# Performance work log

Hardware: AMD Instinct MI355X
Metric: run time of the kernel (lower is better)

The kernel has to match this reference:

```python
import jax, jax.numpy as jnp
import numpy as np

S, B, T = 16, 32, 64        # max_sents, batch, max_tokens
V, E, H = 50000, 256, 256   # vocab, embed_size, gru_hidden (n_dim)
NC = 50                     # n_classes


def setup_inputs() -> dict:
    key = jax.random.key(0)
    ks = jax.random.split(key, 30)

    def u(k, shape, s=0.1):
        return jax.random.uniform(k, shape, minval=-s, maxval=s, dtype=jnp.float32)

    return {
        "x": jax.random.randint(ks[0], (S, B, T), 0, V, dtype=jnp.int64),
        "embed": jax.random.normal(ks[1], (V, E), dtype=jnp.float32) * 0.1,
        # word-level bi-GRU (input E, hidden H); gate order r,z,n as in torch
        "wg_Wih_f": u(ks[2], (3 * H, E)), "wg_Whh_f": u(ks[3], (3 * H, H)),
        "wg_bih_f": u(ks[4], (3 * H,)),   "wg_bhh_f": u(ks[5], (3 * H,)),
        "wg_Wih_b": u(ks[6], (3 * H, E)), "wg_Whh_b": u(ks[7], (3 * H, H)),
        "wg_bih_b": u(ks[8], (3 * H,)),   "wg_bhh_b": u(ks[9], (3 * H,)),
        "word_W": u(ks[10], (2 * H, 2 * H)),
        "word_b": u(ks[11], (2 * H, 1)),
        "word_proj": u(ks[12], (2 * H, 1)),
        # sentence-level bi-GRU (input 2H, hidden H)
        "sg_Wih_f": u(ks[13], (3 * H, 2 * H)), "sg_Whh_f": u(ks[14], (3 * H, H)),
        "sg_bih_f": u(ks[15], (3 * H,)),       "sg_bhh_f": u(ks[16], (3 * H,)),
        "sg_Wih_b": u(ks[17], (3 * H, 2 * H)), "sg_Whh_b": u(ks[18], (3 * H, H)),
        "sg_bih_b": u(ks[19], (3 * H,)),       "sg_bhh_b": u(ks[20], (3 * H,)),
        "sent_W": u(ks[21], (2 * H, 2 * H)),
        "sent_b": u(ks[22], (2 * H, 1)),
        "sent_proj": u(ks[23], (2 * H, 1)),
        "fin_W": u(ks[24], (NC, 2 * H)),
        "fin_b": u(ks[25], (NC,)),
        "state_word": jnp.zeros((2, B, H), dtype=jnp.float32),
        "state_sent": jnp.zeros((2, B, H), dtype=jnp.float32),
    }


def _gru_dir(x, h0, Wih, Whh, bih, bhh, reverse=False):
    # x: [T, B, in]; returns hidden states [T, B, H] (in original time order)
    xp = jnp.einsum('tbe,ge->tbg', x, Wih) + bih  # precompute input projections

    def step(h, xt):
        g = h @ Whh.T + bhh
        xr, xz, xn = jnp.split(xt, 3, axis=-1)
        hr, hz, hn = jnp.split(g, 3, axis=-1)
        r = jax.nn.sigmoid(xr + hr)
        z = jax.nn.sigmoid(xz + hz)
        n = jnp.tanh(xn + r * hn)
        h = (1.0 - z) * n + z * h
        return h, h

    _, hs = jax.lax.scan(step, h0, xp, reverse=reverse)
    return hs


def _bigru(x, h0, Wf, Hf, bif, bhf, Wb, Hb, bib, bhb):
    f = _gru_dir(x, h0[0], Wf, Hf, bif, bhf, reverse=False)
    b = _gru_dir(x, h0[1], Wb, Hb, bib, bhb, reverse=True)
    return jnp.concatenate([f, b], axis=-1)  # [T, B, 2H]


def _attn_pool(out, W, b, proj):
    # out: [T, B, 2H]; batch_matmul_bias(tanh) -> batch_matmul -> softmax over T -> weighted sum
    squish = jnp.tanh(jnp.einsum('tbh,hk->tbk', out, W) + b[:, 0])  # [T,B,2H]
    scores = jnp.einsum('tbk,k->tb', squish, proj[:, 0])            # [T,B]
    a = jax.nn.softmax(scores, axis=0)                              # softmax over seq
    return jnp.einsum('tb,tbh->bh', a, out)                         # [B,2H]


def reference(x, embed,
              wg_Wih_f, wg_Whh_f, wg_bih_f, wg_bhh_f,
              wg_Wih_b, wg_Whh_b, wg_bih_b, wg_bhh_b,
              word_W, word_b, word_proj,
              sg_Wih_f, sg_Whh_f, sg_bih_f, sg_bhh_f,
              sg_Wih_b, sg_Whh_b, sg_bih_b, sg_bhh_b,
              sent_W, sent_b, sent_proj,
              fin_W, fin_b, state_word, state_sent):
    e = embed[x]                         # [S,B,T,E]
    e = jnp.transpose(e, (0, 2, 1, 3))   # [S,T,B,E] (torch code transposes per sentence)

    word_out = jax.vmap(
        lambda xs: _bigru(xs, state_word,
                          wg_Wih_f, wg_Whh_f, wg_bih_f, wg_bhh_f,
                          wg_Wih_b, wg_Whh_b, wg_bih_b, wg_bhh_b)
    )(e)                                 # [S,T,B,2H]

    s = jax.vmap(lambda o: _attn_pool(o, word_W, word_b, word_proj))(word_out)  # [S,B,2H]

    sent_out = _bigru(s, state_sent,
                      sg_Wih_f, sg_Whh_f, sg_bih_f, sg_bhh_f,
                      sg_Wih_b, sg_Whh_b, sg_bih_b, sg_bhh_b)  # [S,B,2H]
    pooled = _attn_pool(sent_out, sent_W, sent_b, sent_proj)   # [B,2H]
    return pooled @ fin_W.T + fin_b                            # [B,NC] logits
```

## Files before the change

### kernel.cpp

```cpp
#include <hip/hip_runtime.h>


typedef float  f32x4  __attribute__((ext_vector_type(4)));
typedef int    i32x4  __attribute__((ext_vector_type(4)));
typedef __bf16 bf16x8 __attribute__((ext_vector_type(8)));

#define DEVINL static __device__ __forceinline__

DEVINL unsigned short f2bf(float f) {
    unsigned int x = __builtin_bit_cast(unsigned int, f);
    x = x + 0x7fffu + ((x >> 16) & 1u);
    return (unsigned short)(x >> 16);
}
DEVINL float bf2f(unsigned short u) {
    unsigned int x = ((unsigned int)u) << 16;
    return __builtin_bit_cast(float, x);
}
DEVINL float bfe16(unsigned int v, int hi) {
    return bf2f((unsigned short)(hi ? (v >> 16) : (v & 0xffffu)));
}
DEVINL float sigm(float x) { return __builtin_amdgcn_rcpf(1.f + __expf(-x)); }
DEVINL float tanh_(float x) {
    x = fminf(fmaxf(x, -20.f), 20.f);
    float e = __expf(-2.f * x);
    return (1.f - e) * __builtin_amdgcn_rcpf(1.f + e);
}
DEVINL void mfma16(f32x4& acc, i32x4 a, i32x4 b) {
    acc = __builtin_amdgcn_mfma_f32_16x16x32_bf16(
        __builtin_bit_cast(bf16x8, a), __builtin_bit_cast(bf16x8, b), acc, 0, 0, 0);
}
DEVINL f32x4 zero4() { f32x4 v = {0.f, 0.f, 0.f, 0.f}; return v; }

#define O_WPWF    ((size_t)0)
#define O_WPWB    ((size_t)1048576)
#define O_WPSGIH  ((size_t)2097152)
#define O_WPSHHF  ((size_t)3670016)
#define O_WPSHHB  ((size_t)4063232)
#define O_WPWW    ((size_t)4456448)
#define O_WPSW    ((size_t)4980736)
#define O_BIASWF  ((size_t)5505024)
#define O_BIASWB  ((size_t)5509120)
#define O_BIHCAT  ((size_t)5513216)
#define O_WOUT    ((size_t)5519360)
#define O_SCORESW ((size_t)39073792)
#define O_SSFRAG  ((size_t)39204864)
#define O_XPSENT  ((size_t)39729152)
#define O_SOFRAG  ((size_t)42874880)
#define O_SCORESS ((size_t)43399168)
#define WS_NEED_B ((size_t)43401216)
#define O_XPW     ((size_t)43401216)
#define WS_NEED_A ((size_t)144064512)

__global__ void k_prep(const float* wihf, const float* whhf,
                       const float* wihb, const float* whhb,
                       const float* sgihf, const float* sgihb,
                       const float* sghhf, const float* sghhb,
                       const float* wordW, const float* sentW,
                       const float* bihf, const float* bhhf,
                       const float* bihb, const float* bhhb,
                       const float* sgbihf, const float* sgbihb,
                       const float* sgbhhf, const float* sgbhhb,
                       unsigned short* Wpwf, unsigned short* Wpwb,
                       unsigned short* Wpsgih,
                       unsigned short* WpshhF, unsigned short* WpshhB,
                       unsigned short* WpwW, unsigned short* WpsW,
                       float* biasWf, float* biasWb, float* bihCat)
{
    const int tid0 = blockIdx.x * blockDim.x + threadIdx.x;
    const int nth  = gridDim.x * blockDim.x;

    for (int idx = tid0; idx < 2 * 524288; idx += nth) {
        int d = idx >> 19, sidx = idx & 524287;
        int j = sidx & 7, chunk = sidx >> 3;
        int lane = chunk & 63, nk = chunk >> 6;
        int kf = nk & 15, nf = nk >> 4;
        int n = nf * 16 + (lane & 15);
        int k = kf * 32 + (lane >> 4) * 8 + j;
        const float* Wih = d ? wihb : wihf;
        const float* Whh = d ? whhb : whhf;
        int g4 = n >> 8, jj = n & 255;
        float v = 0.f;
        if (k < 256) {
            if (g4 == 0) v = Wih[jj * 256 + k];
            else if (g4 == 1) v = Wih[(256 + jj) * 256 + k];
            else if (g4 == 2) v = Wih[(512 + jj) * 256 + k];
        } else {
            int kk = k - 256;
            if (g4 == 0) v = Whh[jj * 256 + kk];
            else if (g4 == 1) v = Whh[(256 + jj) * 256 + kk];
            else if (g4 == 3) v = Whh[(512 + jj) * 256 + kk];
        }
        (d ? Wpwb : Wpwf)[sidx] = f2bf(v);
    }
    for (int idx = tid0; idx < 786432; idx += nth) {
        int j = idx & 7, chunk = idx >> 3;
        int lane = chunk & 63, nk = chunk >> 6;
        int kf = nk & 15, nf = nk >> 4;
        int n = nf * 16 + (lane & 15);
        int k = kf * 32 + (lane >> 4) * 8 + j;
        float v = (n < 768) ? sgihf[n * 512 + k] : sgihb[(n - 768) * 512 + k];
        Wpsgih[idx] = f2bf(v);
    }
    for (int idx = tid0; idx < 2 * 196608; idx += nth) {
        int d = idx >= 196608;
        int sidx = d ? idx - 196608 : idx;
        int j = sidx & 7, chunk = sidx >> 3;
        int lane = chunk & 63, nk = chunk >> 6;
        int kf = nk & 7, nf = nk >> 3;
        int n = nf * 16 + (lane & 15);
        int k = kf * 32 + (lane >> 4) * 8 + j;
        float v = (d ? sghhb : sghhf)[n * 256 + k];
        (d ? WpshhB : WpshhF)[sidx] = f2bf(v);
    }
    for (int idx = tid0; idx < 2 * 262144; idx += nth) {
        int d = idx >> 18, sidx = idx & 262143;
        int j = sidx & 7, chunk = sidx >> 3;
        int lane = chunk & 63, nk = chunk >> 6;
        int kf = nk & 15, nf = nk >> 4;
        int n = nf * 16 + (lane & 15);
        int k = kf * 32 + (lane >> 4) * 8 + j;
        float v = (d ? sentW : wordW)[k * 512 + n];
        (d ? WpsW : WpwW)[sidx] = f2bf(v);
    }
    for (int idx = tid0; idx < 2048; idx += nth) {
        int d = idx >> 10, i = idx & 1023;
        int g4 = i >> 8, j = i & 255;
        const float* bi = d ? bihb : bihf;
        const float* bh = d ? bhhb : bhhf;
        float v = (g4 == 0) ? bi[j] + bh[j]
                : (g4 == 1) ? bi[256 + j] + bh[256 + j]
                : (g4 == 2) ? bi[512 + j] : bh[512 + j];
        (d ? biasWb : biasWf)[i] = v;
    }
    for (int idx = tid0; idx < 1536; idx += nth) {
        int d = idx >= 768, j = d ? idx - 768 : idx;
        const float* bi = d ? sgbihb : sgbihf;
        const float* bh = d ? sgbhhb : sgbhhf;
        bihCat[idx] = bi[j] + ((j < 512) ? bh[j] : 0.f);
    }
}

__global__ __launch_bounds__(512, 2)
void k_xpw(const int* xg, const float* embed,
           const unsigned short* Wpwf_u, const unsigned short* Wpwb_u,
           const float* biasWf, const float* biasWb, unsigned short* xpw)
{
    __shared__ unsigned short Ebuf[2][16][256];
    const int tid = threadIdx.x, lane = tid & 63, w = tid >> 6;
    const int cid = blockIdx.x;
    const int tq = cid & 3, bh = (cid >> 2) & 1, dir = (cid >> 3) & 1, s = cid >> 4;
    const int t0 = tq * 16;
    const i32x4* Wp = (const i32x4*)(dir ? Wpwb_u : Wpwf_u);
    const float* biasW = dir ? biasWb : biasWf;
    const int b = lane & 15, rsub = lane >> 4;

    i32x4 A[3][2][8];
#pragma unroll
    for (int g = 0; g < 3; ++g)
#pragma unroll
        for (int q = 0; q < 2; ++q)
#pragma unroll
            for (int kk = 0; kk < 8; ++kk)
                A[g][q][kk] = Wp[((g * 16 + w * 2 + q) * 16 + kk) * 64 + lane];

    unsigned int biasp[3][2][2];
#pragma unroll
    for (int g = 0; g < 3; ++g)
#pragma unroll
        for (int q = 0; q < 2; ++q) {
            const int j0 = g * 256 + (w * 2 + q) * 16 + rsub * 4;
            biasp[g][q][0] = (unsigned)f2bf(biasW[j0]) |
                             ((unsigned)f2bf(biasW[j0 + 1]) << 16);
            biasp[g][q][1] = (unsigned)f2bf(biasW[j0 + 2]) |
                             ((unsigned)f2bf(biasW[j0 + 3]) << 16);
        }

    const int sb = tid >> 5, sc = tid & 31;
    const int tokrow = (s * 32 + bh * 16 + sb) * 64;
    const int sdst = sb * 512 + ((sc * 16) ^ ((sb & 7) << 4));

#define STAGE_E(BUF, T)                                                       \
    {                                                                         \
        const int tok = xg[tokrow + (T)];                                     \
        const f32x4* src = (const f32x4*)(embed + (size_t)tok * 256 + sc * 8);\
        f32x4 e0 = src[0], e1 = src[1];                                       \
        i32x4 pk;                                                             \
        pk.x = (int)((unsigned)f2bf(e0.x) | ((unsigned)f2bf(e0.y) << 16));    \
        pk.y = (int)((unsigned)f2bf(e0.z) | ((unsigned)f2bf(e0.w) << 16));    \
        pk.z = (int)((unsigned)f2bf(e1.x) | ((unsigned)f2bf(e1.y) << 16));    \
        pk.w = (int)((unsigned)f2bf(e1.z) | ((unsigned)f2bf(e1.w) << 16));    \
        *(i32x4*)((char*)&Ebuf[BUF][0][0] + sdst) = pk;                       \
    }

    STAGE_E(0, t0);
    const size_t chain = (size_t)((s * 2 + dir) * 2 + bh);
    char* const xpBase = (char*)xpw + chain * 1572864 +
                         (size_t)(rsub * 128 + b * 8);

    for (int tl = 0; tl < 16; ++tl) {
        __syncthreads();
        const int t = t0 + tl, cur = tl & 1, nxt = cur ^ 1;
        if (tl < 15) STAGE_E(nxt, t + 1);

        f32x4 acc[3][2];
#pragma unroll
        for (int g = 0; g < 3; ++g) { acc[g][0] = zero4(); acc[g][1] = zero4(); }
#pragma unroll
        for (int kk = 0; kk < 8; ++kk) {
            const int roff = b * 512 + ((kk * 64 + rsub * 16) ^ ((b & 7) << 4));
            i32x4 eb = *(const i32x4*)((const char*)&Ebuf[cur][0][0] + roff);
            mfma16(acc[0][0], A[0][0][kk], eb); mfma16(acc[0][1], A[0][1][kk], eb);
            mfma16(acc[1][0], A[1][0][kk], eb); mfma16(acc[1][1], A[1][1][kk], eb);
            mfma16(acc[2][0], A[2][0][kk], eb); mfma16(acc[2][1], A[2][1][kk], eb);
        }
        char* ob = xpBase + (size_t)t * 24576;
#pragma unroll
        for (int g = 0; g < 3; ++g)
#pragma unroll
            for (int q = 0; q < 2; ++q) {
                unsigned short us[4];
#pragma unroll
                for (int i = 0; i < 4; ++i)
                    us[i] = f2bf(acc[g][q][i] + bfe16(biasp[g][q][i >> 1], i & 1));
                uint2 pk;
                pk.x = (unsigned)us[0] | ((unsigned)us[1] << 16);
                pk.y = (unsigned)us[2] | ((unsigned)us[3] << 16);
                *(uint2*)(ob + g * 8192 + (w * 2 + q) * 512) = pk;
            }
    }
#undef STAGE_E
}

__global__ __launch_bounds__(512, 2)
void k_gru_wordA(const float* stateW,
                 const unsigned short* Wpwf_u, const unsigned short* Wpwb_u,
                 const float* biasWf, const float* biasWb,
                 const unsigned short* xpw, unsigned short* wout)
{
    __shared__ unsigned short Hbuf[2][16][256];
    const int tid = threadIdx.x, lane = tid & 63, w = tid >> 6;
    const int cid = blockIdx.x, bh = cid & 1, dir = (cid >> 1) & 1, s = cid >> 2;
    const i32x4* Wp = (const i32x4*)(dir ? Wpwb_u : Wpwf_u);
    const float* biasW = dir ? biasWb : biasWf;
    const int b = lane & 15, rsub = lane >> 4;
    const int gmap[3] = {0, 1, 3};

    i32x4 A[3][2][8];
#pragma unroll
    for (int g = 0; g < 3; ++g)
#pragma unroll
        for (int q = 0; q < 2; ++q)
#pragma unroll
            for (int kk = 0; kk < 8; ++kk)
                A[g][q][kk] =
                    Wp[((gmap[g] * 16 + w * 2 + q) * 16 + 8 + kk) * 64 + lane];

    unsigned int bhnp[2][2];
    float hreg[2][4];
#pragma unroll
    for (int q = 0; q < 2; ++q) {
        const int j0 = (w * 2 + q) * 16 + rsub * 4;
        f32x4 h0 = *(const f32x4*)(stateW + dir * 8192 + (bh * 16 + b) * 256 + j0);
        bhnp[q][0] = (unsigned)f2bf(biasW[768 + j0]) |
                     ((unsigned)f2bf(biasW[768 + j0 + 1]) << 16);
        bhnp[q][1] = (unsigned)f2bf(biasW[768 + j0 + 2]) |
                     ((unsigned)f2bf(biasW[768 + j0 + 3]) << 16);
        hreg[q][0] = h0.x; hreg[q][1] = h0.y; hreg[q][2] = h0.z; hreg[q][3] = h0.w;
        uint2 pk;
        pk.x = (unsigned)f2bf(h0.x) | ((unsigned)f2bf(h0.y) << 16);
        pk.y = (unsigned)f2bf(h0.z) | ((unsigned)f2bf(h0.w) << 16);
        const int boff = b * 512 + (((w * 2 + q) * 32 + rsub * 8) ^ ((b & 7) << 4));
        *(uint2*)((char*)&Hbuf[0][0][0] + boff) = pk;
    }
    const size_t chain = (size_t)((s * 2 + dir) * 2 + bh);
    const char* const xpBase = (const char*)xpw + chain * 1572864 +
                               (size_t)(rsub * 128 + b * 8);

    for (int ti = 0; ti < 64; ++ti) {
        __syncthreads();
        const int t = dir ? 63 - ti : ti;
        const int cur = ti & 1, nxt = cur ^ 1;

        uint2 xpv[3][2];
        const char* xb = xpBase + (size_t)t * 24576;
#pragma unroll
        for (int g = 0; g < 3; ++g)
#pragma unroll
            for (int q = 0; q < 2; ++q)
                xpv[g][q] = *(const uint2*)(xb + g * 8192 + (w * 2 + q) * 512);

        f32x4 acc[3][2];
#pragma unroll
        for (int g = 0; g < 3; ++g) { acc[g][0] = zero4(); acc[g][1] = zero4(); }
#pragma unroll
        for (int kk = 0; kk < 8; ++kk) {
            const int roff = b * 512 + ((kk * 64 + rsub * 16) ^ ((b & 7) << 4));
            i32x4 hb = *(const i32x4*)((const char*)&Hbuf[cur][0][0] + roff);
            mfma16(acc[0][0], A[0][0][kk], hb); mfma16(acc[0][1], A[0][1][kk], hb);
            mfma16(acc[1][0], A[1][0][kk], hb); mfma16(acc[1][1], A[1][1][kk], hb);
            mfma16(acc[2][0], A[2][0][kk], hb); mfma16(acc[2][1], A[2][1][kk], hb);
        }
        const int r = (s * 64 + t) * 32 + bh * 16 + b;
#pragma unroll
        for (int q = 0; q < 2; ++q) {
            unsigned short us[4];
#pragma unroll
            for (int i = 0; i < 4; ++i) {
                const unsigned xr = (i < 2) ? xpv[0][q].x : xpv[0][q].y;
                const unsigned xz = (i < 2) ? xpv[1][q].x : xpv[1][q].y;
                const unsigned xn = (i < 2) ? xpv[2][q].x : xpv[2][q].y;
                float rv = sigm(bfe16(xr, i & 1) + acc[0][q][i]);
                float zv = sigm(bfe16(xz, i & 1) + acc[1][q][i]);
                float nv = tanh_(bfe16(xn, i & 1) +
                                 rv * (acc[2][q][i] + bfe16(bhnp[q][i >> 1], i & 1)));
                float h = (1.f - zv) * nv + zv * hreg[q][i];
                hreg[q][i] = h;
                us[i] = f2bf(h);
            }
            uint2 pk;
            pk.x = (unsigned)us[0] | ((unsigned)us[1] << 16);
            pk.y = (unsigned)us[2] | ((unsigned)us[3] << 16);
            const int boff = b * 512 + (((w * 2 + q) * 32 + rsub * 8) ^ ((b & 7) << 4));
            *(uint2*)((char*)&Hbuf[nxt][0][0] + boff) = pk;
            const int hcol = dir * 256 + (w * 2 + q) * 16 + rsub * 4;
            const int widx = (((r >> 4) * 16 + (hcol >> 5)) * 64 + (r & 15) +
                              ((hcol >> 3) & 3) * 16) * 8 + (hcol & 7);
            *(uint2*)(wout + widx) = pk;
        }
    }
}

DEVINL void prefetchE(unsigned short (*Ab)[512], const int* xg, const float* embed,
                      int s, int t, int tid)
{
    const int brow = tid >> 5, c = tid & 31;
    const int tok = xg[(s * 32 + brow) * 64 + t];
    const f32x4* src = (const f32x4*)(embed + (size_t)tok * 256) + c * 2;
    f32x4 f0 = src[0], f1 = src[1];
    i32x4 pk;
    pk.x = (int)((unsigned)f2bf(f0.x) | ((unsigned)f2bf(f0.y) << 16));
    pk.y = (int)((unsigned)f2bf(f0.z) | ((unsigned)f2bf(f0.w) << 16));
    pk.z = (int)((unsigned)f2bf(f1.x) | ((unsigned)f2bf(f1.y) << 16));
    pk.w = (int)((unsigned)f2bf(f1.z) | ((unsigned)f2bf(f1.w) << 16));
    int kbyte = (c * 16) ^ ((brow & 7) << 4);
    *(i32x4*)((char*)&Ab[brow][0] + kbyte) = pk;
}

__global__ __launch_bounds__(1024, 4)
void k_gru_word(const int* xg, const float* embed, const float* stateW,
                const unsigned short* Wpwf_u, const unsigned short* Wpwb_u,
                const float* biasWf, const float* biasWb,
                unsigned short* wout)
{
    __shared__ unsigned short Abuf[2][32][512];
    const int tid = threadIdx.x, lane = tid & 63, w = tid >> 6;
    const int cid = blockIdx.x, s = cid >> 1, dir = cid & 1;
    const i32x4* Wp = (const i32x4*)(dir ? Wpwb_u : Wpwf_u);
    const float* bias = dir ? biasWb : biasWf;

    const int j = w * 16 + (lane & 15);
    float hreg[2][4];
#pragma unroll
    for (int mf = 0; mf < 2; ++mf)
#pragma unroll
        for (int i = 0; i < 4; ++i) {
            int b = mf * 16 + (lane >> 4) * 4 + i;
            float h0 = stateW[dir * 8192 + b * 256 + j];
            hreg[mf][i] = h0;
            int byteoff = ((256 + j) * 2) ^ ((b & 7) << 4);
            *(unsigned short*)((char*)&Abuf[0][b][0] + byteoff) = f2bf(h0);
        }
    const int tfirst = dir ? 63 : 0;
    prefetchE(Abuf[0], xg, embed, s, tfirst, tid);

    const float br = bias[j], bz = bias[256 + j];
    const float bxn = bias[512 + j], bhn = bias[768 + j];

    for (int ti = 0; ti < 64; ++ti) {
        __syncthreads();
        const int t = dir ? 63 - ti : ti;
        const int cur = ti & 1, nxt = cur ^ 1;
        if (ti < 63) prefetchE(Abuf[nxt], xg, embed, s, dir ? t - 1 : t + 1, tid);

        f32x4 acc[4][2];
#pragma unroll
        for (int g = 0; g < 4; ++g) { acc[g][0] = zero4(); acc[g][1] = zero4(); }

        i32x4 bbuf[3][3];
#define LOADB_W(KF, DST)                                                     \
        {                                                                    \
            const int gX = ((KF) < 8) ? 32 : 48;                             \
            DST[0] = Wp[((0 + w)  * 16 + (KF)) * 64 + lane];                 \
            DST[1] = Wp[((16 + w) * 16 + (KF)) * 64 + lane];                 \
            DST[2] = Wp[((gX + w) * 16 + (KF)) * 64 + lane];                 \
        }
        LOADB_W(0, bbuf[0]);
        LOADB_W(1, bbuf[1]);
#pragma unroll
        for (int kf = 0; kf < 16; ++kf) {
            if (kf < 14) LOADB_W(kf + 2, bbuf[(kf + 2) % 3]);
            const int row0 = lane & 15;
            const int boff = (kf * 64 + (lane >> 4) * 16) ^ ((row0 & 7) << 4);
            i32x4 a0 = *(const i32x4*)((const char*)&Abuf[cur][row0][0] + boff);
            i32x4 a1 = *(const i32x4*)((const char*)&Abuf[cur][16 + row0][0] + boff);
            const i32x4* bc = bbuf[kf % 3];
            mfma16(acc[0][0], a0, bc[0]); mfma16(acc[0][1], a1, bc[0]);
            mfma16(acc[1][0], a0, bc[1]); mfma16(acc[1][1], a1, bc[1]);
            if (kf < 8) { mfma16(acc[2][0], a0, bc[2]);
                          mfma16(acc[2][1], a1, bc[2]); }
            else        { mfma16(acc[3][0], a0, bc[2]);
                          mfma16(acc[3][1], a1, bc[2]); }
        }
#undef LOADB_W
#pragma unroll
        for (int mf = 0; mf < 2; ++mf)
#pragma unroll
            for (int i = 0; i < 4; ++i) {
                const int b = mf * 16 + (lane >> 4) * 4 + i;
                float rv = sigm(acc[0][mf][i] + br);
                float zv = sigm(acc[1][mf][i] + bz);
                float nv = tanh_(acc[2][mf][i] + bxn + rv * (acc[3][mf][i] + bhn));
                float hnew = (1.f - zv) * nv + zv * hreg[mf][i];
                hreg[mf][i] = hnew;
                unsigned short hb = f2bf(hnew);
                int byteoff = ((256 + j) * 2) ^ ((b & 7) << 4);
                *(unsigned short*)((char*)&Abuf[nxt][b][0] + byteoff) = hb;
                int r = (s * 64 + t) * 32 + b;
                int hcol = dir * 256 + j;
                wout[(((r >> 4) * 16 + (hcol >> 5)) * 64 + (r & 15) +
                      ((hcol >> 3) & 3) * 16) * 8 + (hcol & 7)] = hb;
            }
    }
}

__global__ __launch_bounds__(1024, 4)
void k_attn_score2(const unsigned short* Afrag_u, const unsigned short* Wp_u,
                   const float* wb, const float* wp, float* scores)
{
    __shared__ i32x4 Wl[2][16][64];
    const int tid = threadIdx.x, lane = tid & 63, w = tid >> 6;
    const int rblk = blockIdx.x * 16 + w;
    const i32x4* A = (const i32x4*)Afrag_u;
    const i32x4* Wg = (const i32x4*)Wp_u;

    i32x4 a[16];
#pragma unroll
    for (int kf = 0; kf < 16; ++kf) a[kf] = A[(rblk * 16 + kf) * 64 + lane];

    i32x4* wl0 = &Wl[0][0][0];
    i32x4* wl1 = &Wl[1][0][0];
    wl0[tid] = Wg[tid];

    float partial[4] = {};
    for (int nf = 0; nf < 32; ++nf) {
        __syncthreads();
        if (nf < 31) {
            i32x4* dst = (nf & 1) ? wl0 : wl1;
            dst[tid] = Wg[(nf + 1) * 1024 + tid];
        }
        const i32x4* cur = (nf & 1) ? wl1 : wl0;
        f32x4 acc0 = zero4(), acc1 = zero4();
#pragma unroll
        for (int kf = 0; kf < 16; kf += 2) {
            mfma16(acc0, a[kf],     cur[kf * 64 + lane]);
            mfma16(acc1, a[kf + 1], cur[(kf + 1) * 64 + lane]);
        }
        const int n = nf * 16 + (lane & 15);
        const float wbn = wb[n], wpn = wp[n];
#pragma unroll
        for (int i = 0; i < 4; ++i)
            partial[i] += tanh_(acc0[i] + acc1[i] + wbn) * wpn;
    }
#pragma unroll
    for (int i = 0; i < 4; ++i) {
        float v = partial[i];
        v += __shfl_xor(v, 1); v += __shfl_xor(v, 2);
        v += __shfl_xor(v, 4); v += __shfl_xor(v, 8);
        if ((lane & 15) == 0)
            scores[rblk * 16 + (lane >> 4) * 4 + i] = v;
    }
}

__global__ void k_attn_score_small(const unsigned short* Afrag_u,
                                   const unsigned short* Wp_u,
                                   const float* wb, const float* wp, float* scores)
{
    const int tid = threadIdx.x, lane = tid & 63, w = tid >> 6;
    const int rblk = blockIdx.x * 4 + w;
    const i32x4* A = (const i32x4*)Afrag_u;
    const i32x4* Wp = (const i32x4*)Wp_u;
    i32x4 a[16];
#pragma unroll
    for (int kf = 0; kf < 16; ++kf) a[kf] = A[(rblk * 16 + kf) * 64 + lane];

    float partial[4] = {};
    for (int nf = 0; nf < 32; ++nf) {
        f32x4 acc0 = zero4(), acc1 = zero4();
#pragma unroll
        for (int kf = 0; kf < 16; kf += 2) {
            mfma16(acc0, a[kf],     Wp[(nf * 16 + kf) * 64 + lane]);
            mfma16(acc1, a[kf + 1], Wp[(nf * 16 + kf + 1) * 64 + lane]);
        }
        const int n = nf * 16 + (lane & 15);
        const float wbn = wb[n], wpn = wp[n];
#pragma unroll
        for (int i = 0; i < 4; ++i)
            partial[i] += tanh_(acc0[i] + acc1[i] + wbn) * wpn;
    }
#pragma unroll
    for (int i = 0; i < 4; ++i) {
        float v = partial[i];
        v += __shfl_xor(v, 1); v += __shfl_xor(v, 2);
        v += __shfl_xor(v, 4); v += __shfl_xor(v, 8);
        if ((lane & 15) == 0)
            scores[rblk * 16 + (lane >> 4) * 4 + i] = v;
    }
}

__global__ void k_word_pool(const float* scores, const unsigned short* wout,
                            unsigned short* ssFrag)
{
    __shared__ float aL[64];
    __shared__ float part[4][64][8];
    const int tid = threadIdx.x, l = tid & 63, w = tid >> 6;
    const int bid = blockIdx.x;
    const int s = bid >> 5, b = bid & 31;
    if (w == 0) {
        float sc = scores[s * 2048 + l * 32 + b];
        float m = sc;
#pragma unroll
        for (int d = 1; d < 64; d <<= 1) m = fmaxf(m, __shfl_xor(m, d));
        float e = __expf(sc - m), sum = e;
#pragma unroll
        for (int d = 1; d < 64; d <<= 1) sum += __shfl_xor(sum, d);
        aL[l] = e * __builtin_amdgcn_rcpf(sum);
    }
    __syncthreads();

    float acc[8] = {};
    const i32x4* WO = (const i32x4*)wout;
    for (int tt = 0; tt < 16; ++tt) {
        const int t = w * 16 + tt;
        float at = aL[t];
        int cidx = ((s * 128 + t * 2 + (b >> 4)) * 16 + (l >> 2)) * 64 +
                   (b & 15) + (l & 3) * 16;
        i32x4 ch = WO[cidx];
        acc[0] += at * bf2f((unsigned short)((unsigned)ch.x & 0xffffu));
        acc[1] += at * bf2f((unsigned short)((unsigned)ch.x >> 16));
        acc[2] += at * bf2f((unsigned short)((unsigned)ch.y & 0xffffu));
        acc[3] += at * bf2f((unsigned short)((unsigned)ch.y >> 16));
        acc[4] += at * bf2f((unsigned short)((unsigned)ch.z & 0xffffu));
        acc[5] += at * bf2f((unsigned short)((unsigned)ch.z >> 16));
        acc[6] += at * bf2f((unsigned short)((unsigned)ch.w & 0xffffu));
        acc[7] += at * bf2f((unsigned short)((unsigned)ch.w >> 16));
    }
#pragma unroll
    for (int q = 0; q < 8; ++q) part[w][l][q] = acc[q];
    __syncthreads();
    if (w == 0) {
        float fin[8];
#pragma unroll
        for (int q = 0; q < 8; ++q)
            fin[q] = part[0][l][q] + part[1][l][q] + part[2][l][q] + part[3][l][q];
        i32x4 pk;
        pk.x = (int)((unsigned)f2bf(fin[0]) | ((unsigned)f2bf(fin[1]) << 16));
        pk.y = (int)((unsigned)f2bf(fin[2]) | ((unsigned)f2bf(fin[3]) << 16));
        pk.z = (int)((unsigned)f2bf(fin[4]) | ((unsigned)f2bf(fin[5]) << 16));
        pk.w = (int)((unsigned)f2bf(fin[6]) | ((unsigned)f2bf(fin[7]) << 16));
        const int r2 = s * 32 + b;
        int cidx2 = ((r2 >> 4) * 16 + (l >> 2)) * 64 + (r2 & 15) + (l & 3) * 16;
        ((i32x4*)ssFrag)[cidx2] = pk;
    }
}

__global__ void k_sgih(const unsigned short* ssFrag_u, const unsigned short* Wp_u,
                       const float* bihCat, float* xpSent)
{
    const int tid = threadIdx.x, lane = tid & 63, w = tid >> 6;
    const int rblk = blockIdx.x, ncl = blockIdx.y;
    const i32x4* A = (const i32x4*)ssFrag_u;
    const i32x4* Wp = (const i32x4*)Wp_u;
    i32x4 a[16];
#pragma unroll
    for (int kf = 0; kf < 16; ++kf) a[kf] = A[(rblk * 16 + kf) * 64 + lane];
#pragma unroll
    for (int nfl = 0; nfl < 4; ++nfl) {
        const int nfg = ncl * 16 + w * 4 + nfl;
        f32x4 acc = zero4();
#pragma unroll
        for (int kf = 0; kf < 16; ++kf)
            mfma16(acc, a[kf], Wp[(nfg * 16 + kf) * 64 + lane]);
        const int n = nfg * 16 + (lane & 15);
        const float bb = bihCat[n];
        const int dir = n >= 768, ng = n - dir * 768;
        const int g = ng >> 8, jj = ng & 255;
#pragma unroll
        for (int i = 0; i < 4; ++i) {
            int row = rblk * 16 + (lane >> 4) * 4 + i;
            int s = row >> 5, b = row & 31;
            xpSent[(((dir * 2 + (b >> 4)) * 16 + s) * 12288) +
                   (g * 256 + jj) * 16 + (b & 15)] = acc[i] + bb;
        }
    }
}

DEVINL void gload16(const void* gsrc, void* ldst) {
    __builtin_amdgcn_global_load_lds(
        (const __attribute__((address_space(1))) unsigned int*)gsrc,
        (__attribute__((address_space(3))) unsigned int*)ldst, 16, 0, 0);
}

__global__ __launch_bounds__(512)
void k_gru_sentA(const float* stateS, const unsigned short* WpF_u,
                 const unsigned short* WpB_u, const float* bhhf, const float* bhhb,
                 const float* xpSent, unsigned short* soFrag)
{
    __shared__ unsigned short Abuf[2][16][256];
    __shared__ float xpLs[2][12288];
    const int tid = threadIdx.x, lane = tid & 63, w = tid >> 6;
    const int cid = blockIdx.x, bh = cid & 1, dir = cid >> 1;
    const i32x4* Wp = (const i32x4*)(dir ? WpB_u : WpF_u);
    const float* bhh = dir ? bhhb : bhhf;

    i32x4 B[3][2][8];
#pragma unroll
    for (int g = 0; g < 3; ++g)
#pragma unroll
        for (int q = 0; q < 2; ++q)
#pragma unroll
            for (int kk = 0; kk < 8; ++kk)
                B[g][q][kk] = Wp[((g * 16 + w * 2 + q) * 8 + kk) * 64 + lane];

    float bhn[2];
    float hreg[2][4];
#pragma unroll
    for (int q = 0; q < 2; ++q) {
        const int j = (w * 2 + q) * 16 + (lane & 15);
        bhn[q] = bhh[512 + j];
#pragma unroll
        for (int i = 0; i < 4; ++i) {
            const int b = 4 * (lane >> 4) + i;
            float h0 = stateS[dir * 8192 + (bh * 16 + b) * 256 + j];
            hreg[q][i] = h0;
            int byteoff = b * 512 + ((j * 2) ^ ((b & 7) << 4));
            *(unsigned short*)((char*)&Abuf[0][0][0] + byteoff) = f2bf(h0);
        }
    }
    const size_t xbase = (size_t)((dir * 2 + bh) * 16) * 49152;
    const int sfirst = dir ? 15 : 0;
#pragma unroll
    for (int c = 0; c < 6; ++c)
        gload16((const char*)xpSent + xbase + (size_t)sfirst * 49152 +
                    ((w * 6 + c) * 64 + lane) * 16,
                (char*)&xpLs[0][0] + (w * 6 + c) * 1024);

    for (int si = 0; si < 16; ++si) {
        __syncthreads();
        const int s = dir ? 15 - si : si;
        const int cur = si & 1, nxt = cur ^ 1;
        if (si < 15) {
            const int sn = dir ? s - 1 : s + 1;
#pragma unroll
            for (int c = 0; c < 6; ++c)
                gload16((const char*)xpSent + xbase + (size_t)sn * 49152 +
                            ((w * 6 + c) * 64 + lane) * 16,
                        (char*)&xpLs[nxt][0] + (w * 6 + c) * 1024);
        }
        f32x4 acc[3][2];
#pragma unroll
        for (int g = 0; g < 3; ++g) { acc[g][0] = zero4(); acc[g][1] = zero4(); }
#pragma unroll
        for (int kk = 0; kk < 8; ++kk) {
            const int row = lane & 15;
            const int boff = (kk * 64 + (lane >> 4) * 16) ^ ((row & 7) << 4);
            i32x4 a = *(const i32x4*)((const char*)&Abuf[cur][row][0] + boff);
#pragma unroll
            for (int g = 0; g < 3; ++g) {
                mfma16(acc[g][0], a, B[g][0][kk]);
                mfma16(acc[g][1], a, B[g][1][kk]);
            }
        }
#pragma unroll
        for (int q = 0; q < 2; ++q) {
            const int j = (w * 2 + q) * 16 + (lane & 15);
            f32x4 xr = *(const f32x4*)((const char*)&xpLs[cur][0] +
                        ((0 * 256 + j) * 16 + 4 * (lane >> 4)) * 4);
            f32x4 xz = *(const f32x4*)((const char*)&xpLs[cur][0] +
                        ((1 * 256 + j) * 16 + 4 * (lane >> 4)) * 4);
            f32x4 xn = *(const f32x4*)((const char*)&xpLs[cur][0] +
                        ((2 * 256 + j) * 16 + 4 * (lane >> 4)) * 4);
#pragma unroll
            for (int i = 0; i < 4; ++i) {
                const int b = 4 * (lane >> 4) + i;
                float rv = sigm(xr[i] + acc[0][q][i]);
                float zv = sigm(xz[i] + acc[1][q][i]);
                float nv = tanh_(xn[i] + rv * (acc[2][q][i] + bhn[q]));
                float hnew = (1.f - zv) * nv + zv * hreg[q][i];
                hreg[q][i] = hnew;
                unsigned short hb = f2bf(hnew);
                int byteoff = b * 512 + ((j * 2) ^ ((b & 7) << 4));
                *(unsigned short*)((char*)&Abuf[nxt][0][0] + byteoff) = hb;
                const int r2 = s * 32 + bh * 16 + b;
                const int hcol = dir * 256 + j;
                soFrag[(((r2 >> 4) * 16 + (hcol >> 5)) * 64 + (r2 & 15) +
                        ((hcol >> 3) & 3) * 16) * 8 + (hcol & 7)] = hb;
            }
        }
    }
}

__global__ void k_sent_pool_fin(const float* scoresS, const unsigned short* soFrag,
                                const float* finW, const float* finb, float* out)
{
    __shared__ float aL[16];
    __shared__ float pooled[512];
    __shared__ float part[4][64];
    const int l = threadIdx.x;
    const int b = blockIdx.x;

    if (l < 64) {
        float sc = (l < 16) ? scoresS[l * 32 + b] : -1e30f;
        float m = sc;
#pragma unroll
        for (int d = 1; d < 16; d <<= 1) m = fmaxf(m, __shfl_xor(m, d));
        float e = (l < 16) ? __expf(sc - m) : 0.f;
        float sum = e;
#pragma unroll
        for (int d = 1; d < 16; d <<= 1) sum += __shfl_xor(sum, d);
        if (l < 16) aL[l] = e * __builtin_amdgcn_rcpf(sum);
    }
    __syncthreads();

    if (l < 64) {
        float acc[8] = {};
        const i32x4* SO = (const i32x4*)soFrag;
        for (int si = 0; si < 16; ++si) {
            float as = aL[si];
            int r2 = si * 32 + b;
            int cidx = ((r2 >> 4) * 16 + (l >> 2)) * 64 + (r2 & 15) + (l & 3) * 16;
            i32x4 ch = SO[cidx];
            acc[0] += as * bf2f((unsigned short)((unsigned)ch.x & 0xffffu));
            acc[1] += as * bf2f((unsigned short)((unsigned)ch.x >> 16));
            acc[2] += as * bf2f((unsigned short)((unsigned)ch.y & 0xffffu));
            acc[3] += as * bf2f((unsigned short)((unsigned)ch.y >> 16));
            acc[4] += as * bf2f((unsigned short)((unsigned)ch.z & 0xffffu));
            acc[5] += as * bf2f((unsigned short)((unsigned)ch.z >> 16));
            acc[6] += as * bf2f((unsigned short)((unsigned)ch.w & 0xffffu));
            acc[7] += as * bf2f((unsigned short)((unsigned)ch.w >> 16));
        }
#pragma unroll
        for (int q = 0; q < 8; ++q) pooled[l * 8 + q] = acc[q];
    }
    __syncthreads();
    {
        const int c = l & 63, kq = l >> 6;
        float v = 0.f;
        if (c < 50) {
            const float* wrow = finW + c * 512 + kq * 128;
            const float* pp = pooled + kq * 128;
            for (int k = 0; k < 128; ++k) v += pp[k] * wrow[k];
        }
        part[kq][c] = v;
    }
    __syncthreads();
    if (l < 50)
        out[b * 50 + l] = finb[l] + part[0][l] + part[1][l] + part[2][l] + part[3][l];
}

extern "C" void kernel_launch(void* const* d_in, const int* in_sizes, int n_in,
                              void* d_out, int out_size, void* d_ws, size_t ws_size,
                              hipStream_t stream)
{
    if (ws_size < WS_NEED_B) return;
    const int bigA = (ws_size >= WS_NEED_A) ? 1 : 0;

    const int*   x      = (const int*)d_in[0];
    const float* embed  = (const float*)d_in[1];
    const float* wgWihF = (const float*)d_in[2];
    const float* wgWhhF = (const float*)d_in[3];
    const float* wgBihF = (const float*)d_in[4];
    const float* wgBhhF = (const float*)d_in[5];
    const float* wgWihB = (const float*)d_in[6];
    const float* wgWhhB = (const float*)d_in[7];
    const float* wgBihB = (const float*)d_in[8];
    const float* wgBhhB = (const float*)d_in[9];
    const float* wordW  = (const float*)d_in[10];
    const float* wordB  = (const float*)d_in[11];
    const float* wordP  = (const float*)d_in[12];
    const float* sgWihF = (const float*)d_in[13];
    const float* sgWhhF = (const float*)d_in[14];
    const float* sgBihF = (const float*)d_in[15];
    const float* sgBhhF = (const float*)d_in[16];
    const float* sgWihB = (const float*)d_in[17];
    const float* sgWhhB = (const float*)d_in[18];
    const float* sgBihB = (const float*)d_in[19];
    const float* sgBhhB = (const float*)d_in[20];
    const float* sentWm = (const float*)d_in[21];
    const float* sentB  = (const float*)d_in[22];
    const float* sentP  = (const float*)d_in[23];
    const float* finW   = (const float*)d_in[24];
    const float* finB   = (const float*)d_in[25];
    const float* stateW = (const float*)d_in[26];
    const float* stateS = (const float*)d_in[27];

    char* ws = (char*)d_ws;
    unsigned short* Wpwf   = (unsigned short*)(ws + O_WPWF);
    unsigned short* Wpwb   = (unsigned short*)(ws + O_WPWB);
    unsigned short* Wpsgih = (unsigned short*)(ws + O_WPSGIH);
    unsigned short* WpshhF = (unsigned short*)(ws + O_WPSHHF);
    unsigned short* WpshhB = (unsigned short*)(ws + O_WPSHHB);
    unsigned short* WpwW   = (unsigned short*)(ws + O_WPWW);
    unsigned short* WpsW   = (unsigned short*)(ws + O_WPSW);
    float* biasWf  = (float*)(ws + O_BIASWF);
    float* biasWb  = (float*)(ws + O_BIASWB);
    float* bihCat  = (float*)(ws + O_BIHCAT);
    unsigned short* wout   = (unsigned short*)(ws + O_WOUT);
    float* scoresW = (float*)(ws + O_SCORESW);
    unsigned short* ssFrag = (unsigned short*)(ws + O_SSFRAG);
    float* xpSent  = (float*)(ws + O_XPSENT);
    unsigned short* soFrag = (unsigned short*)(ws + O_SOFRAG);
    float* scoresS = (float*)(ws + O_SCORESS);
    unsigned short* xpw    = (unsigned short*)(ws + O_XPW);

    k_prep<<<512, 256, 0, stream>>>(wgWihF, wgWhhF, wgWihB, wgWhhB,
                                    sgWihF, sgWihB, sgWhhF, sgWhhB,
                                    wordW, sentWm,
                                    wgBihF, wgBhhF, wgBihB, wgBhhB,
                                    sgBihF, sgBihB, sgBhhF, sgBhhB,
                                    Wpwf, Wpwb, Wpsgih, WpshhF, WpshhB,
                                    WpwW, WpsW, biasWf, biasWb, bihCat);

    if (bigA) {
        k_xpw<<<256, 512, 0, stream>>>(x, embed, Wpwf, Wpwb, biasWf, biasWb, xpw);
        k_gru_wordA<<<64, 512, 0, stream>>>(stateW, Wpwf, Wpwb, biasWf, biasWb,
                                            xpw, wout);
    } else {
        k_gru_word<<<32, 1024, 0, stream>>>(x, embed, stateW, Wpwf, Wpwb,
                                            biasWf, biasWb, wout);
    }

    k_attn_score2<<<128, 1024, 0, stream>>>(wout, WpwW, wordB, wordP, scoresW);
    k_word_pool<<<512, 256, 0, stream>>>(scoresW, wout, ssFrag);

    k_sgih<<<dim3(32, 6), 256, 0, stream>>>(ssFrag, Wpsgih, bihCat, xpSent);
    k_gru_sentA<<<4, 512, 0, stream>>>(stateS, WpshhF, WpshhB, sgBhhF, sgBhhB,
                                       xpSent, soFrag);

    k_attn_score_small<<<8, 256, 0, stream>>>(soFrag, WpsW, sentB, sentP, scoresS);
    k_sent_pool_fin<<<32, 256, 0, stream>>>(scoresS, soFrag, finW, finB,
                                            (float*)d_out);
}
```

Measured before the change: 445.2 us.

## Double waves per block in recurrent GRU kernels, one 16-column tile per wave

The word-level and sentence-level recurrent GRU kernels now launch 1024 threads (16 waves) instead of 512. Each wave handles one 16-wide hidden tile rather than two, which halves the serial MFMA chain and gate math per wave on every time step. This also halves each wave's register-resident weight fragments. The cost is a larger block barrier each step and lower occupancy, since only one block fits per CU. The change also switches f2bf to the native bf16 conversion and rewrites the hidden-state update as nv + z*(h-nv).

```diff
diff --git a/kernel.cpp b/kernel.cpp
--- a/kernel.cpp
+++ b/kernel.cpp
@@ -8,9 +8,8 @@
 #define DEVINL static __device__ __forceinline__
 
 DEVINL unsigned short f2bf(float f) {
-    unsigned int x = __builtin_bit_cast(unsigned int, f);
-    x = x + 0x7fffu + ((x >> 16) & 1u);
-    return (unsigned short)(x >> 16);
+    __bf16 b = (__bf16)f;
+    return __builtin_bit_cast(unsigned short, b);
 }
 DEVINL float bf2f(unsigned short u) {
     unsigned int x = ((unsigned int)u) << 16;
@@ -231,7 +230,7 @@
 #undef STAGE_E
 }
 
-__global__ __launch_bounds__(512, 2)
+__global__ __launch_bounds__(1024)
 void k_gru_wordA(const float* stateW,
                  const unsigned short* Wpwf_u, const unsigned short* Wpwb_u,
                  const float* biasWf, const float* biasWb,
@@ -245,31 +244,28 @@
     const int b = lane & 15, rsub = lane >> 4;
     const int gmap[3] = {0, 1, 3};
 
-    i32x4 A[3][2][8];
+    i32x4 A[3][8];
 #pragma unroll
     for (int g = 0; g < 3; ++g)
 #pragma unroll
-        for (int q = 0; q < 2; ++q)
-#pragma unroll
-            for (int kk = 0; kk < 8; ++kk)
-                A[g][q][kk] =
-                    Wp[((gmap[g] * 16 + w * 2 + q) * 16 + 8 + kk) * 64 + lane];
-
-    unsigned int bhnp[2][2];
-    float hreg[2][4];
-#pragma unroll
-    for (int q = 0; q < 2; ++q) {
-        const int j0 = (w * 2 + q) * 16 + rsub * 4;
+        for (int kk = 0; kk < 8; ++kk)
+            A[g][kk] = Wp[((gmap[g] * 16 + w) * 16 + 8 + kk) * 64 + lane];
+
+    const int j0 = w * 16 + rsub * 4;
+    unsigned int bhnp[2];
+    bhnp[0] = (unsigned)f2bf(biasW[768 + j0]) |
+              ((unsigned)f2bf(biasW[768 + j0 + 1]) << 16);
+    bhnp[1] = (unsigned)f2bf(biasW[768 + j0 + 2]) |
+              ((unsigned)f2bf(biasW[768 + j0 + 3]) << 16);
+
+    const int boff = b * 512 + ((w * 32 + rsub * 8) ^ ((b & 7) << 4));
+    float hreg[4];
+    {
         f32x4 h0 = *(const f32x4*)(stateW + dir * 8192 + (bh * 16 + b) * 256 + j0);
-        bhnp[q][0] = (unsigned)f2bf(biasW[768 + j0]) |
-                     ((unsigned)f2bf(biasW[768 + j0 + 1]) << 16);
-        bhnp[q][1] = (unsigned)f2bf(biasW[768 + j0 + 2]) |
-                     ((unsigned)f2bf(biasW[768 + j0 + 3]) << 16);
-        hreg[q][0] = h0.x; hreg[q][1] = h0.y; hreg[q][2] = h0.z; hreg[q][3] = h0.w;
+        hreg[0] = h0.x; hreg[1] = h0.y; hreg[2] = h0.z; hreg[3] = h0.w;
         uint2 pk;
         pk.x = (unsigned)f2bf(h0.x) | ((unsigned)f2bf(h0.y) << 16);
         pk.y = (unsigned)f2bf(h0.z) | ((unsigned)f2bf(h0.w) << 16);
-        const int boff = b * 512 + (((w * 2 + q) * 32 + rsub * 8) ^ ((b & 7) << 4));
         *(uint2*)((char*)&Hbuf[0][0][0] + boff) = pk;
     }
     const size_t chain = (size_t)((s * 2 + dir) * 2 + bh);
@@ -281,52 +277,46 @@
         const int t = dir ? 63 - ti : ti;
         const int cur = ti & 1, nxt = cur ^ 1;
 
-        uint2 xpv[3][2];
+        uint2 xpv[3];
         const char* xb = xpBase + (size_t)t * 24576;
 #pragma unroll
         for (int g = 0; g < 3; ++g)
-#pragma unroll
-            for (int q = 0; q < 2; ++q)
-                xpv[g][q] = *(const uint2*)(xb + g * 8192 + (w * 2 + q) * 512);
-
-        f32x4 acc[3][2];
-#pragma unroll
-        for (int g = 0; g < 3; ++g) { acc[g][0] = zero4(); acc[g][1] = zero4(); }
+            xpv[g] = *(const uint2*)(xb + g * 8192 + w * 512);
+
+        f32x4 acc[3];
+#pragma unroll
+        for (int g = 0; g < 3; ++g) acc[g] = zero4();
 #pragma unroll
         for (int kk = 0; kk < 8; ++kk) {
             const int roff = b * 512 + ((kk * 64 + rsub * 16) ^ ((b & 7) << 4));
             i32x4 hb = *(const i32x4*)((const char*)&Hbuf[cur][0][0] + roff);
-            mfma16(acc[0][0], A[0][0][kk], hb); mfma16(acc[0][1], A[0][1][kk], hb);
-            mfma16(acc[1][0], A[1][0][kk], hb); mfma16(acc[1][1], A[1][1][kk], hb);
-            mfma16(acc[2][0], A[2][0][kk], hb); mfma16(acc[2][1], A[2][1][kk], hb);
+            mfma16(acc[0], A[0][kk], hb);
+            mfma16(acc[1], A[1][kk], hb);
+            mfma16(acc[2], A[2][kk], hb);
         }
         const int r = (s * 64 + t) * 32 + bh * 16 + b;
-#pragma unroll
-        for (int q = 0; q < 2; ++q) {
-            unsigned short us[4];
-#pragma unroll
-            for (int i = 0; i < 4; ++i) {
-                const unsigned xr = (i < 2) ? xpv[0][q].x : xpv[0][q].y;
-                const unsigned xz = (i < 2) ? xpv[1][q].x : xpv[1][q].y;
-                const unsigned xn = (i < 2) ? xpv[2][q].x : xpv[2][q].y;
-                float rv = sigm(bfe16(xr, i & 1) + acc[0][q][i]);
-                float zv = sigm(bfe16(xz, i & 1) + acc[1][q][i]);
-                float nv = tanh_(bfe16(xn, i & 1) +
-                                 rv * (acc[2][q][i] + bfe16(bhnp[q][i >> 1], i & 1)));
-                float h = (1.f - zv) * nv + zv * hreg[q][i];
-                hreg[q][i] = h;
-                us[i] = f2bf(h);
-            }
-            uint2 pk;
-            pk.x = (unsigned)us[0] | ((unsigned)us[1] << 16);
-            pk.y = (unsigned)us[2] | ((unsigned)us[3] << 16);
-            const int boff = b * 512 + (((w * 2 + q) * 32 + rsub * 8) ^ ((b & 7) << 4));
-            *(uint2*)((char*)&Hbuf[nxt][0][0] + boff) = pk;
-            const int hcol = dir * 256 + (w * 2 + q) * 16 + rsub * 4;
-            const int widx = (((r >> 4) * 16 + (hcol >> 5)) * 64 + (r & 15) +
-                              ((hcol >> 3) & 3) * 16) * 8 + (hcol & 7);
-            *(uint2*)(wout + widx) = pk;
-        }
+        unsigned short us[4];
+#pragma unroll
+        for (int i = 0; i < 4; ++i) {
+            const unsigned xr = (i < 2) ? xpv[0].x : xpv[0].y;
+            const unsigned xz = (i < 2) ? xpv[1].x : xpv[1].y;
+            const unsigned xn = (i < 2) ? xpv[2].x : xpv[2].y;
+            float rv = sigm(bfe16(xr, i & 1) + acc[0][i]);
+            float zv = sigm(bfe16(xz, i & 1) + acc[1][i]);
+            float nv = tanh_(bfe16(xn, i & 1) +
+                             rv * (acc[2][i] + bfe16(bhnp[i >> 1], i & 1)));
+            float h = nv + zv * (hreg[i] - nv);
+            hreg[i] = h;
+            us[i] = f2bf(h);
+        }
+        uint2 pk;
+        pk.x = (unsigned)us[0] | ((unsigned)us[1] << 16);
+        pk.y = (unsigned)us[2] | ((unsigned)us[3] << 16);
+        *(uint2*)((char*)&Hbuf[nxt][0][0] + boff) = pk;
+        const int hcol = dir * 256 + j0;
+        const int widx = (((r >> 4) * 16 + (hcol >> 5)) * 64 + (r & 15) +
+                          ((hcol >> 3) & 3) * 16) * 8 + (hcol & 7);
+        *(uint2*)(wout + widx) = pk;
     }
 }
 
@@ -610,7 +600,7 @@
         (__attribute__((address_space(3))) unsigned int*)ldst, 16, 0, 0);
 }
 
-__global__ __launch_bounds__(512)
+__global__ __launch_bounds__(1024)
 void k_gru_sentA(const float* stateS, const unsigned short* WpF_u,
                  const unsigned short* WpB_u, const float* bhhf, const float* bhhb,
                  const float* xpSent, unsigned short* soFrag)
@@ -622,37 +612,31 @@
     const i32x4* Wp = (const i32x4*)(dir ? WpB_u : WpF_u);
     const float* bhh = dir ? bhhb : bhhf;
 
-    i32x4 B[3][2][8];
+    i32x4 B[3][8];
 #pragma unroll
     for (int g = 0; g < 3; ++g)
 #pragma unroll
-        for (int q = 0; q < 2; ++q)
-#pragma unroll
-            for (int kk = 0; kk < 8; ++kk)
-                B[g][q][kk] = Wp[((g * 16 + w * 2 + q) * 8 + kk) * 64 + lane];
-
-    float bhn[2];
-    float hreg[2][4];
-#pragma unroll
-    for (int q = 0; q < 2; ++q) {
-        const int j = (w * 2 + q) * 16 + (lane & 15);
-        bhn[q] = bhh[512 + j];
-#pragma unroll
-        for (int i = 0; i < 4; ++i) {
-            const int b = 4 * (lane >> 4) + i;
-            float h0 = stateS[dir * 8192 + (bh * 16 + b) * 256 + j];
-            hreg[q][i] = h0;
-            int byteoff = b * 512 + ((j * 2) ^ ((b & 7) << 4));
-            *(unsigned short*)((char*)&Abuf[0][0][0] + byteoff) = f2bf(h0);
-        }
+        for (int kk = 0; kk < 8; ++kk)
+            B[g][kk] = Wp[((g * 16 + w) * 8 + kk) * 64 + lane];
+
+    const int j = w * 16 + (lane & 15);
+    const float bhn = bhh[512 + j];
+    float hreg[4];
+#pragma unroll
+    for (int i = 0; i < 4; ++i) {
+        const int b = 4 * (lane >> 4) + i;
+        float h0 = stateS[dir * 8192 + (bh * 16 + b) * 256 + j];
+        hreg[i] = h0;
+        int byteoff = b * 512 + ((j * 2) ^ ((b & 7) << 4));
+        *(unsigned short*)((char*)&Abuf[0][0][0] + byteoff) = f2bf(h0);
     }
     const size_t xbase = (size_t)((dir * 2 + bh) * 16) * 49152;
     const int sfirst = dir ? 15 : 0;
 #pragma unroll
-    for (int c = 0; c < 6; ++c)
+    for (int c = 0; c < 3; ++c)
         gload16((const char*)xpSent + xbase + (size_t)sfirst * 49152 +
-                    ((w * 6 + c) * 64 + lane) * 16,
-                (char*)&xpLs[0][0] + (w * 6 + c) * 1024);
+                    ((w * 3 + c) * 64 + lane) * 16,
+                (char*)&xpLs[0][0] + (w * 3 + c) * 1024);
 
     for (int si = 0; si < 16; ++si) {
         __syncthreads();
@@ -661,50 +645,44 @@
         if (si < 15) {
             const int sn = dir ? s - 1 : s + 1;
 #pragma unroll
-            for (int c = 0; c < 6; ++c)
+            for (int c = 0; c < 3; ++c)
                 gload16((const char*)xpSent + xbase + (size_t)sn * 49152 +
-                            ((w * 6 + c) * 64 + lane) * 16,
-                        (char*)&xpLs[nxt][0] + (w * 6 + c) * 1024);
-        }
-        f32x4 acc[3][2];
-#pragma unroll
-        for (int g = 0; g < 3; ++g) { acc[g][0] = zero4(); acc[g][1] = zero4(); }
+                            ((w * 3 + c) * 64 + lane) * 16,
+                        (char*)&xpLs[nxt][0] + (w * 3 + c) * 1024);
+        }
+        f32x4 acc[3];
+#pragma unroll
+        for (int g = 0; g < 3; ++g) acc[g] = zero4();
 #pragma unroll
         for (int kk = 0; kk < 8; ++kk) {
             const int row = lane & 15;
             const int boff = (kk * 64 + (lane >> 4) * 16) ^ ((row & 7) << 4);
             i32x4 a = *(const i32x4*)((const char*)&Abuf[cur][row][0] + boff);
-#pragma unroll
-            for (int g = 0; g < 3; ++g) {
-                mfma16(acc[g][0], a, B[g][0][kk]);
-                mfma16(acc[g][1], a, B[g][1][kk]);
-            }
-        }
-#pragma unroll
-        for (int q = 0; q < 2; ++q) {
-            const int j = (w * 2 + q) * 16 + (lane & 15);
-            f32x4 xr = *(const f32x4*)((const char*)&xpLs[cur][0] +
-                        ((0 * 256 + j) * 16 + 4 * (lane >> 4)) * 4);
-            f32x4 xz = *(const f32x4*)((const char*)&xpLs[cur][0] +
-                        ((1 * 256 + j) * 16 + 4 * (lane >> 4)) * 4);
-            f32x4 xn = *(const f32x4*)((const char*)&xpLs[cur][0] +
-                        ((2 * 256 + j) * 16 + 4 * (lane >> 4)) * 4);
-#pragma unroll
-            for (int i = 0; i < 4; ++i) {
-                const int b = 4 * (lane >> 4) + i;
-                float rv = sigm(xr[i] + acc[0][q][i]);
-                float zv = sigm(xz[i] + acc[1][q][i]);
-                float nv = tanh_(xn[i] + rv * (acc[2][q][i] + bhn[q]));
-                float hnew = (1.f - zv) * nv + zv * hreg[q][i];
-                hreg[q][i] = hnew;
-                unsigned short hb = f2bf(hnew);
-                int byteoff = b * 512 + ((j * 2) ^ ((b & 7) << 4));
-                *(unsigned short*)((char*)&Abuf[nxt][0][0] + byteoff) = hb;
-                const int r2 = s * 32 + bh * 16 + b;
-                const int hcol = dir * 256 + j;
-                soFrag[(((r2 >> 4) * 16 + (hcol >> 5)) * 64 + (r2 & 15) +
-                        ((hcol >> 3) & 3) * 16) * 8 + (hcol & 7)] = hb;
-            }
+            mfma16(acc[0], a, B[0][kk]);
+            mfma16(acc[1], a, B[1][kk]);
+            mfma16(acc[2], a, B[2][kk]);
+        }
+        f32x4 xr = *(const f32x4*)((const char*)&xpLs[cur][0] +
+                    ((0 * 256 + j) * 16 + 4 * (lane >> 4)) * 4);
+        f32x4 xz = *(const f32x4*)((const char*)&xpLs[cur][0] +
+                    ((1 * 256 + j) * 16 + 4 * (lane >> 4)) * 4);
+        f32x4 xn = *(const f32x4*)((const char*)&xpLs[cur][0] +
+                    ((2 * 256 + j) * 16 + 4 * (lane >> 4)) * 4);
+#pragma unroll
+        for (int i = 0; i < 4; ++i) {
+            const int b = 4 * (lane >> 4) + i;
+            float rv = sigm(xr[i] + acc[0][i]);
+            float zv = sigm(xz[i] + acc[1][i]);
+            float nv = tanh_(xn[i] + rv * (acc[2][i] + bhn));
+            float hnew = nv + zv * (hreg[i] - nv);
+            hreg[i] = hnew;
+            unsigned short hb = f2bf(hnew);
+            int byteoff = b * 512 + ((j * 2) ^ ((b & 7) << 4));
+            *(unsigned short*)((char*)&Abuf[nxt][0][0] + byteoff) = hb;
+            const int r2 = s * 32 + bh * 16 + b;
+            const int hcol = dir * 256 + j;
+            soFrag[(((r2 >> 4) * 16 + (hcol >> 5)) * 64 + (r2 & 15) +
+                    ((hcol >> 3) & 3) * 16) * 8 + (hcol & 7)] = hb;
         }
     }
 }
@@ -832,8 +810,8 @@
 
     if (bigA) {
         k_xpw<<<256, 512, 0, stream>>>(x, embed, Wpwf, Wpwb, biasWf, biasWb, xpw);
-        k_gru_wordA<<<64, 512, 0, stream>>>(stateW, Wpwf, Wpwb, biasWf, biasWb,
-                                            xpw, wout);
+        k_gru_wordA<<<64, 1024, 0, stream>>>(stateW, Wpwf, Wpwb, biasWf, biasWb,
+                                             xpw, wout);
     } else {
         k_gru_word<<<32, 1024, 0, stream>>>(x, embed, stateW, Wpwf, Wpwb,
                                             biasWf, biasWb, wout);
@@ -843,8 +821,8 @@
     k_word_pool<<<512, 256, 0, stream>>>(scoresW, wout, ssFrag);
 
     k_sgih<<<dim3(32, 6), 256, 0, stream>>>(ssFrag, Wpsgih, bihCat, xpSent);
-    k_gru_sentA<<<4, 512, 0, stream>>>(stateS, WpshhF, WpshhB, sgBhhF, sgBhhB,
-                                       xpSent, soFrag);
+    k_gru_sentA<<<4, 1024, 0, stream>>>(stateS, WpshhF, WpshhB, sgBhhF, sgBhhB,
+                                        xpSent, soFrag);
 
     k_attn_score_small<<<8, 256, 0, stream>>>(soFrag, WpsW, sentB, sentP, scoresS);
     k_sent_pool_fin<<<32, 256, 0, stream>>>(scoresS, soFrag, finW, finB,
```

New measurement: 501.0 us. 1.13x slower.
